# Kernel tuning notes

Measured on AMD Instinct MI355X. Metric: run time of the kernel, lower is better.

The kernel has to match this reference:

```python
import jax, jax.numpy as jnp
import numpy as np

B, S, D, DFF = 8, 2048, 1024, 4096

def setup_inputs() -> dict:
    key = jax.random.key(0)
    ks = jax.random.split(key, 11)
    s = 0.02
    return {
        "x":  jax.random.normal(ks[0], (B, S, D), dtype=jnp.float32),
        "Wq": jax.random.normal(ks[1], (D, D), dtype=jnp.float32) * s,
        "bq": jnp.zeros((D,), dtype=jnp.float32),
        "Wk": jax.random.normal(ks[2], (D, D), dtype=jnp.float32) * s,
        "bk": jnp.zeros((D,), dtype=jnp.float32),
        "Wv": jax.random.normal(ks[3], (D, D), dtype=jnp.float32) * s,
        "bv": jnp.zeros((D,), dtype=jnp.float32),
        "W1": jax.random.normal(ks[4], (DFF, D), dtype=jnp.float32) * s,
        "b1": jnp.zeros((DFF,), dtype=jnp.float32),
        "W2": jax.random.normal(ks[5], (D, DFF), dtype=jnp.float32) * s,
        "b2": jnp.zeros((D,), dtype=jnp.float32),
    }

def reference(x, Wq, bq, Wk, bk, Wv, bv, W1, b1, W2, b2):
    # qkv projections (torch Linear: x @ W.T + b)
    q = jnp.einsum('bsd,ed->bse', x, Wq) + bq
    k = jnp.einsum('bsd,ed->bse', x, Wk) + bk
    v = jnp.einsum('bsd,ed->bse', x, Wv) + bv
    # single-head scaled dot-product attention with causal mask (decoder=True)
    scale = 1.0 / jnp.sqrt(jnp.asarray(q.shape[-1], q.dtype))
    scores = jnp.einsum('bqd,bkd->bqk', q, k) * scale  # (B,S,S)
    causal = jnp.tril(jnp.ones((scores.shape[-2], scores.shape[-1]), dtype=bool))
    scores = jnp.where(causal, scores, jnp.asarray(-jnp.inf, scores.dtype))
    attn = jax.nn.softmax(scores, axis=-1)
    attn_out = jnp.einsum('bqk,bkd->bqd', attn, v)
    # MLP: linear_2(gelu(linear_1(.)))  — exact (erf) GELU as in torch default
    h = jax.nn.gelu(jnp.einsum('bsd,fd->bsf', attn_out, W1) + b1, approximate=False)
    return jnp.einsum('bsf,df->bsd', h, W2) + b2
```

## Files before the change

### kernel.cpp

```cpp
#include <hip/hip_runtime.h>
#include <hip/hip_bf16.h>

#define NB   8
#define SS   2048
#define DD   1024
#define DFFN 4096
#define MTOT (NB*SS)

typedef unsigned short u16;
typedef __attribute__((ext_vector_type(4))) float f32x4;
typedef __attribute__((ext_vector_type(8))) short bf16x8;
typedef __attribute__((ext_vector_type(4))) unsigned short u16x4;
typedef __attribute__((ext_vector_type(8))) unsigned short u16x8;

__device__ __forceinline__ u16 f2bf(float f) {
  union { float f; unsigned u; } c; c.f = f;
  unsigned r = c.u + 0x7FFFu + ((c.u >> 16) & 1u);
  return (u16)(r >> 16);
}

__device__ __forceinline__ void gload16(const void* g, void* l) {
  __builtin_amdgcn_global_load_lds(
      (const __attribute__((address_space(1))) void*)(unsigned long long)g,
      (__attribute__((address_space(3))) void*)(unsigned)(unsigned long long)l,
      16, 0, 0);
}

template<int EBIAS, int EGELU, int ESCALE, int EROWSCALE, int OUTMODE, int ETRANS, int CSKIP, int CK>
__global__ __launch_bounds__(512, 2)
void gemm256(const u16* __restrict__ A, const u16* __restrict__ B,
             const float* __restrict__ bias, const float* __restrict__ rowscale,
             void* __restrict__ C,
             int M, int N, int K, int lda, int ldb, int ldc, float scale,
             long long sA, long long sB, long long sC, int sRS)
{
  __shared__ __align__(1024) u16 smem[65536];

  const int nwg = gridDim.x * gridDim.y;
  const int orig = blockIdx.y * gridDim.x + blockIdx.x;
  const int q = nwg >> 3, r = nwg & 7;
  const int xcd = orig & 7, pos = orig >> 3;
  const int wg = (xcd < r ? xcd * (q + 1) : r * (q + 1) + (xcd - r) * q) + pos;
  const int bx = wg % gridDim.x, by = wg / gridDim.x;
  const int row0 = by * 256, col0 = bx * 256;
  if (CSKIP && col0 > row0 + 255) return;

  const int z = blockIdx.z;
  A += (size_t)z * sA;
  B += (size_t)z * sB;

  int nkt = K >> 5;
  if (CK) { int lim = (row0 + 256) >> 5; if (lim < nkt) nkt = lim; }

  const int tid  = threadIdx.x;
  const int wid  = tid >> 6;
  const int lane = tid & 63;
  const int wr = wid >> 2, wc = wid & 3;

  const int srow = wid * 16 + (lane >> 2);
  const int sunit = (lane & 3) ^ ((lane >> 3) & 3);
  const char* gA = (const char*)A + ((size_t)(row0 + srow) * lda + sunit * 8) * 2;
  const char* gB = (const char*)B + ((size_t)(col0 + srow) * ldb + sunit * 8) * 2;
  char* lbase = (char*)smem;
  const size_t ldab = (size_t)128 * lda * 2;
  const size_t ldbb = (size_t)128 * ldb * 2;

  #define STAGE(kt) {                                                        \
    char* lb = lbase + ((kt) & 3) * 32768;                                   \
    size_t kb = (size_t)(kt) * 64;                                           \
    gload16(gA + kb,        lb + wid * 1024);                                \
    gload16(gA + kb + ldab, lb + 8192 + wid * 1024);                         \
    gload16(gB + kb,        lb + 16384 + wid * 1024);                        \
    gload16(gB + kb + ldbb, lb + 16384 + 8192 + wid * 1024);                 \
  }

  const int rd_off = (lane & 15) * 64 + ((lane >> 4) & 3) * 16;
  const int xm = ((lane >> 1) & 3) << 4;
  const int aoff = wr * 8192;
  const int boff = 16384 + wc * 4096;

  f32x4 acc[8][4] = {};

  STAGE(0); STAGE(1); STAGE(2);
  asm volatile("s_waitcnt vmcnt(8)" ::: "memory");
  asm volatile("s_barrier" ::: "memory");

  for (int t = 0; t < nkt; ++t) {
    const int cb = (t & 3) * 32768;
    if (t + 3 < nkt) STAGE(t + 3);

    bf16x8 aR[8], bR[4];
#pragma unroll
    for (int m = 0; m < 8; ++m)
      aR[m] = *(const bf16x8*)((const char*)smem + ((cb + aoff + m * 1024 + rd_off) ^ xm));
#pragma unroll
    for (int n = 0; n < 4; ++n)
      bR[n] = *(const bf16x8*)((const char*)smem + ((cb + boff + n * 1024 + rd_off) ^ xm));

    __builtin_amdgcn_s_setprio(1);
#pragma unroll
    for (int m = 0; m < 8; ++m)
#pragma unroll
      for (int n = 0; n < 4; ++n)
        acc[m][n] = __builtin_amdgcn_mfma_f32_16x16x32_bf16(aR[m], bR[n], acc[m][n], 0, 0, 0);
    __builtin_amdgcn_s_setprio(0);

    asm volatile("s_waitcnt vmcnt(8)" ::: "memory");
    asm volatile("s_barrier" ::: "memory");
  }
  #undef STAGE

  const int r4 = (lane >> 4) * 4;
#pragma unroll
  for (int n = 0; n < 4; ++n) {
    const int col = col0 + wc * 64 + n * 16 + (lane & 15);
    float bia = EBIAS ? bias[col] : 0.0f;
#pragma unroll
    for (int m = 0; m < 8; ++m) {
      const int rowb = row0 + wr * 128 + m * 16 + r4;
#pragma unroll
      for (int j = 0; j < 4; ++j) {
        const int row = rowb + j;
        float x = acc[m][n][j];
        if (EBIAS)     x += bia;
        if (ESCALE)    x *= scale;
        if (EROWSCALE) x *= rowscale[z * sRS + row];
        if (EGELU)     x = 0.5f * x * (1.0f + erff(x * 0.70710678118f));
        if (ETRANS) {
          ((u16*)C)[(size_t)(row >> 11) * (DD * SS) + (size_t)col * SS + (row & (SS - 1))] = f2bf(x);
        } else if (OUTMODE == 1) {
          ((float*)C + (size_t)z * sC)[(size_t)row * ldc + col] = x;
        } else if (OUTMODE == 2) {
          ((_Float16*)C + (size_t)z * sC)[(size_t)row * ldc + col] = (_Float16)x;
        } else {
          ((u16*)C + (size_t)z * sC)[(size_t)row * ldc + col] = f2bf(x);
        }
      }
    }
  }
}

__global__ __launch_bounds__(256) void cvt_bf16_k(const float* __restrict__ in, u16* __restrict__ out, int n4) {
  int i = blockIdx.x * blockDim.x + threadIdx.x;
  if (i < n4) {
    float4 v = ((const float4*)in)[i];
    u16x4 o;
    o.x = f2bf(v.x); o.y = f2bf(v.y); o.z = f2bf(v.z); o.w = f2bf(v.w);
    ((u16x4*)out)[i] = o;
  }
}

__global__ __launch_bounds__(256) void softmax_k(u16* __restrict__ sc, float* __restrict__ rinv, int rows0) {
  const int widx = blockIdx.x * 4 + (threadIdx.x >> 6);
  const int lane = threadIdx.x & 63;
  u16* row = sc + (size_t)widx * SS;
  const int L = (widx & (SS - 1)) + 1;
  float mx = -1e30f;
  for (int k = 0; k < 4; ++k) {
    const int j0 = k * 512 + lane * 8;
    if (j0 < L) {
      u16x8 v = *(const u16x8*)(row + j0);
      int lim = L - j0; if (lim > 8) lim = 8;
#pragma unroll
      for (int e = 0; e < 8; ++e) {
        if (e < lim) { union { u16 u; _Float16 h; } c; c.u = v[e]; mx = fmaxf(mx, (float)c.h); }
      }
    }
  }
#pragma unroll
  for (int o = 32; o >= 1; o >>= 1) mx = fmaxf(mx, __shfl_xor(mx, o));
  float s = 0.0f;
  for (int k = 0; k < 4; ++k) {
    const int j0 = k * 512 + lane * 8;
    u16x8 v = *(const u16x8*)(row + j0);
    u16x8 w;
#pragma unroll
    for (int e = 0; e < 8; ++e) {
      const int j = j0 + e;
      float ev = 0.0f;
      if (j < L) { union { u16 u; _Float16 h; } c; c.u = v[e]; ev = __expf((float)c.h - mx); s += ev; }
      w[e] = f2bf(ev);
    }
    *(u16x8*)(row + j0) = w;
  }
#pragma unroll
  for (int o = 32; o >= 1; o >>= 1) s += __shfl_xor(s, o);
  if (lane == 0) rinv[rows0 + widx] = 1.0f / s;
}

extern "C" void kernel_launch(void* const* d_in, const int* in_sizes, int n_in,
                              void* d_out, int out_size, void* d_ws, size_t ws_size,
                              hipStream_t stream) {
  const float* x  = (const float*)d_in[0];
  const float* Wq = (const float*)d_in[1];
  const float* bq = (const float*)d_in[2];
  const float* Wk = (const float*)d_in[3];
  const float* bk = (const float*)d_in[4];
  const float* Wv = (const float*)d_in[5];
  const float* bv = (const float*)d_in[6];
  const float* W1 = (const float*)d_in[7];
  const float* b1 = (const float*)d_in[8];
  const float* W2 = (const float*)d_in[9];
  const float* b2 = (const float*)d_in[10];

  char* ws = (char*)d_ws;
  u16*  xb   = (u16*)(ws);
  u16*  Wqb  = (u16*)(ws + 33554432);
  u16*  Wkb  = (u16*)(ws + 35651584);
  u16*  Wvb  = (u16*)(ws + 37748736);
  u16*  W1b  = (u16*)(ws + 39845888);
  u16*  W2b  = (u16*)(ws + 48234496);
  u16*  Qb   = (u16*)(ws + 56623104);
  u16*  Kb   = (u16*)(ws + 90177536);
  u16*  Vtb  = (u16*)(ws + 123731968);
  float* rinv = (float*)(ws + 157286400);
  u16*  big  = (u16*)(ws + 157351936);
  u16*  att  = xb;

  const size_t base = 157351936ull;
  const size_t avail = ws_size > base ? ws_size - base : 0;
  int GB = 8; while (GB > 1 && (size_t)GB * 8388608ull > avail) GB >>= 1;
  int MC = 8192; while (MC > 2048 && (size_t)MC * 8192ull > avail) MC >>= 1;

  cvt_bf16_k<<<MTOT * DD / 4 / 256, 256, 0, stream>>>(x, xb, MTOT * DD / 4);
  cvt_bf16_k<<<DD * DD / 4 / 256, 256, 0, stream>>>(Wq, Wqb, DD * DD / 4);
  cvt_bf16_k<<<DD * DD / 4 / 256, 256, 0, stream>>>(Wk, Wkb, DD * DD / 4);
  cvt_bf16_k<<<DD * DD / 4 / 256, 256, 0, stream>>>(Wv, Wvb, DD * DD / 4);
  cvt_bf16_k<<<DFFN * DD / 4 / 256, 256, 0, stream>>>(W1, W1b, DFFN * DD / 4);
  cvt_bf16_k<<<DFFN * DD / 4 / 256, 256, 0, stream>>>(W2, W2b, DFFN * DD / 4);

  gemm256<1,0,0,0,0,0,0,0><<<dim3(DD/256, MTOT/256), 512, 0, stream>>>(
      xb, Wqb, bq, nullptr, (void*)Qb, MTOT, DD, DD, DD, DD, DD, 0.f, 0, 0, 0, 0);
  gemm256<1,0,0,0,0,0,0,0><<<dim3(DD/256, MTOT/256), 512, 0, stream>>>(
      xb, Wkb, bk, nullptr, (void*)Kb, MTOT, DD, DD, DD, DD, DD, 0.f, 0, 0, 0, 0);
  gemm256<1,0,0,0,0,1,0,0><<<dim3(DD/256, MTOT/256), 512, 0, stream>>>(
      xb, Wvb, bv, nullptr, (void*)Vtb, MTOT, DD, DD, DD, DD, DD, 0.f, 0, 0, 0, 0);

  for (int b0 = 0; b0 < NB; b0 += GB) {
    gemm256<0,0,1,0,2,0,1,0><<<dim3(SS/256, SS/256, GB), 512, 0, stream>>>(
        Qb + (size_t)b0 * SS * DD, Kb + (size_t)b0 * SS * DD, nullptr, nullptr,
        (void*)big, SS, SS, DD, DD, DD, SS, 0.03125f,
        (long long)SS * DD, (long long)SS * DD, (long long)SS * SS, 0);
    softmax_k<<<GB * SS / 4, 256, 0, stream>>>(big, rinv, b0 * SS);
    gemm256<0,0,0,1,0,0,0,1><<<dim3(DD/256, SS/256, GB), 512, 0, stream>>>(
        big, Vtb + (size_t)b0 * DD * SS, nullptr, rinv + (size_t)b0 * SS,
        (void*)(att + (size_t)b0 * SS * DD), SS, DD, SS, SS, SS, DD, 0.f,
        (long long)SS * SS, (long long)DD * SS, (long long)SS * DD, SS);
  }

  for (int c = 0; c < MTOT / MC; ++c) {
    u16* h = big;
    gemm256<1,1,0,0,0,0,0,0><<<dim3(DFFN/256, MC/256), 512, 0, stream>>>(
        att + (size_t)c * MC * DD, W1b, b1, nullptr, (void*)h,
        MC, DFFN, DD, DD, DD, DFFN, 0.f, 0, 0, 0, 0);
    gemm256<1,0,0,0,1,0,0,0><<<dim3(DD/256, MC/256), 512, 0, stream>>>(
        h, W2b, b2, nullptr, (void*)((float*)d_out + (size_t)c * MC * DD),
        MC, DD, DFFN, DFFN, DFFN, DD, 0.f, 0, 0, 0, 0);
  }
}
```

Before: 812.2 us.

## Split GEMM k-loop into two half-phases and stage epilogue through LDS

```diff
diff --git a/kernel.cpp b/kernel.cpp
--- a/kernel.cpp
+++ b/kernel.cpp
@@ -39,8 +39,8 @@
   const int nwg = gridDim.x * gridDim.y;
   const int orig = blockIdx.y * gridDim.x + blockIdx.x;
   const int q = nwg >> 3, r = nwg & 7;
-  const int xcd = orig & 7, pos = orig >> 3;
-  const int wg = (xcd < r ? xcd * (q + 1) : r * (q + 1) + (xcd - r) * q) + pos;
+  const int xcd = orig & 7, pos0 = orig >> 3;
+  const int wg = (xcd < r ? xcd * (q + 1) : r * (q + 1) + (xcd - r) * q) + pos0;
   const int bx = wg % gridDim.x, by = wg / gridDim.x;
   const int row0 = by * 256, col0 = bx * 256;
   if (CSKIP && col0 > row0 + 255) return;
@@ -65,77 +65,164 @@
   const size_t ldab = (size_t)128 * lda * 2;
   const size_t ldbb = (size_t)128 * ldb * 2;
 
-  #define STAGE(kt) {                                                        \
-    char* lb = lbase + ((kt) & 3) * 32768;                                   \
-    size_t kb = (size_t)(kt) * 64;                                           \
-    gload16(gA + kb,        lb + wid * 1024);                                \
-    gload16(gA + kb + ldab, lb + 8192 + wid * 1024);                         \
-    gload16(gB + kb,        lb + 16384 + wid * 1024);                        \
-    gload16(gB + kb + ldbb, lb + 16384 + 8192 + wid * 1024);                 \
-  }
-
-  const int rd_off = (lane & 15) * 64 + ((lane >> 4) & 3) * 16;
+  #define SHA(t2) { char* lb = lbase + ((t2) & 3) * 32768; size_t kb = (size_t)(t2) * 64; \
+      gload16(gA + kb,        lb + wid * 1024);                                          \
+      gload16(gA + kb + ldab, lb + 8192 + wid * 1024); }
+  #define SHB(t2) { char* lb = lbase + ((t2) & 3) * 32768; size_t kb = (size_t)(t2) * 64; \
+      gload16(gB + kb,        lb + 16384 + wid * 1024);                                   \
+      gload16(gB + kb + ldbb, lb + 16384 + 8192 + wid * 1024); }
+
+  const int fr = lane & 15;
+  const int rd_off = fr * 64 + ((lane >> 4) & 3) * 16;
   const int xm = ((lane >> 1) & 3) << 4;
   const int aoff = wr * 8192;
   const int boff = 16384 + wc * 4096;
 
   f32x4 acc[8][4] = {};
-
-  STAGE(0); STAGE(1); STAGE(2);
+  bf16x8 aLo[4], aHi[4], bb[4];
+
+  SHA(0); SHB(0); SHA(1); SHB(1); SHA(2); SHB(2);
   asm volatile("s_waitcnt vmcnt(8)" ::: "memory");
   asm volatile("s_barrier" ::: "memory");
 
   for (int t = 0; t < nkt; ++t) {
-    const int cb = (t & 3) * 32768;
-    if (t + 3 < nkt) STAGE(t + 3);
-
-    bf16x8 aR[8], bR[4];
-#pragma unroll
-    for (int m = 0; m < 8; ++m)
-      aR[m] = *(const bf16x8*)((const char*)smem + ((cb + aoff + m * 1024 + rd_off) ^ xm));
+    const char* cbuf = (const char*)smem + (t & 3) * 32768;
+#pragma unroll
+    for (int m = 0; m < 4; ++m)
+      aLo[m] = *(const bf16x8*)(cbuf + ((aoff + m * 1024 + rd_off) ^ xm));
 #pragma unroll
     for (int n = 0; n < 4; ++n)
-      bR[n] = *(const bf16x8*)((const char*)smem + ((cb + boff + n * 1024 + rd_off) ^ xm));
-
+      bb[n] = *(const bf16x8*)(cbuf + ((boff + n * 1024 + rd_off) ^ xm));
+    if (t + 3 < nkt) SHA(t + 3);
+    asm volatile("s_barrier" ::: "memory");
     __builtin_amdgcn_s_setprio(1);
 #pragma unroll
-    for (int m = 0; m < 8; ++m)
+    for (int m = 0; m < 4; ++m)
 #pragma unroll
       for (int n = 0; n < 4; ++n)
-        acc[m][n] = __builtin_amdgcn_mfma_f32_16x16x32_bf16(aR[m], bR[n], acc[m][n], 0, 0, 0);
+        acc[m][n] = __builtin_amdgcn_mfma_f32_16x16x32_bf16(aLo[m], bb[n], acc[m][n], 0, 0, 0);
     __builtin_amdgcn_s_setprio(0);
-
+    asm volatile("s_barrier" ::: "memory");
+#pragma unroll
+    for (int m = 0; m < 4; ++m)
+      aHi[m] = *(const bf16x8*)(cbuf + ((aoff + (m + 4) * 1024 + rd_off) ^ xm));
+    if (t + 3 < nkt) SHB(t + 3);
     asm volatile("s_waitcnt vmcnt(8)" ::: "memory");
     asm volatile("s_barrier" ::: "memory");
-  }
-  #undef STAGE
-
+    __builtin_amdgcn_s_setprio(1);
+#pragma unroll
+    for (int m = 0; m < 4; ++m)
+#pragma unroll
+      for (int n = 0; n < 4; ++n)
+        acc[m + 4][n] = __builtin_amdgcn_mfma_f32_16x16x32_bf16(aHi[m], bb[n], acc[m + 4][n], 0, 0, 0);
+    __builtin_amdgcn_s_setprio(0);
+    asm volatile("s_barrier" ::: "memory");
+  }
+  #undef SHA
+  #undef SHB
+
+  asm volatile("s_waitcnt vmcnt(0)" ::: "memory");
+  __syncthreads();
+
+  char* sm = (char*)smem;
   const int r4 = (lane >> 4) * 4;
-#pragma unroll
-  for (int n = 0; n < 4; ++n) {
-    const int col = col0 + wc * 64 + n * 16 + (lane & 15);
-    float bia = EBIAS ? bias[col] : 0.0f;
-#pragma unroll
-    for (int m = 0; m < 8; ++m) {
-      const int rowb = row0 + wr * 128 + m * 16 + r4;
-#pragma unroll
-      for (int j = 0; j < 4; ++j) {
-        const int row = rowb + j;
-        float x = acc[m][n][j];
-        if (EBIAS)     x += bia;
-        if (ESCALE)    x *= scale;
-        if (EROWSCALE) x *= rowscale[z * sRS + row];
-        if (EGELU)     x = 0.5f * x * (1.0f + erff(x * 0.70710678118f));
-        if (ETRANS) {
-          ((u16*)C)[(size_t)(row >> 11) * (DD * SS) + (size_t)col * SS + (row & (SS - 1))] = f2bf(x);
-        } else if (OUTMODE == 1) {
-          ((float*)C + (size_t)z * sC)[(size_t)row * ldc + col] = x;
-        } else if (OUTMODE == 2) {
-          ((_Float16*)C + (size_t)z * sC)[(size_t)row * ldc + col] = (_Float16)x;
-        } else {
-          ((u16*)C + (size_t)z * sC)[(size_t)row * ldc + col] = f2bf(x);
+
+  if (OUTMODE == 1) {
+#pragma unroll
+    for (int p = 0; p < 2; ++p) {
+      if ((wc >> 1) == p) {
+#pragma unroll
+        for (int n = 0; n < 4; ++n) {
+          const int col = col0 + wc * 64 + n * 16 + fr;
+          const int pcol = (wc & 1) * 64 + n * 16 + fr;
+          float bia = EBIAS ? bias[col] : 0.0f;
+#pragma unroll
+          for (int m = 0; m < 8; ++m) {
+#pragma unroll
+            for (int j = 0; j < 4; ++j) {
+              const int line = wr * 128 + m * 16 + r4 + j;
+              float xv = acc[m][n][j];
+              if (EBIAS)     xv += bia;
+              if (ESCALE)    xv *= scale;
+              if (EROWSCALE) xv *= rowscale[z * sRS + row0 + line];
+              if (EGELU)     xv = 0.5f * xv * (1.0f + erff(xv * 0.70710678118f));
+              *(float*)(sm + ((line * 512 + pcol * 4) ^ ((line & 12) << 3))) = xv;
+            }
+          }
         }
       }
+      __syncthreads();
+      float* Cb = (float*)C + (size_t)z * sC;
+#pragma unroll
+      for (int i = 0; i < 16; ++i) {
+        const int o = i * 8192 + tid * 16;
+        const int line = o >> 9, ps = o & 511;
+        f32x4 v = *(const f32x4*)(sm + ((line * 512 + ps) ^ ((line & 12) << 3)));
+        *(f32x4*)((char*)(Cb + (size_t)(row0 + line) * ldc + col0 + p * 128) + ps) = v;
+      }
+      __syncthreads();
+    }
+  } else if (ETRANS) {
+#pragma unroll
+    for (int n = 0; n < 4; ++n) {
+      const int col = col0 + wc * 64 + n * 16 + fr;
+      const int line = wc * 64 + n * 16 + fr;
+      float bia = EBIAS ? bias[col] : 0.0f;
+#pragma unroll
+      for (int m = 0; m < 8; ++m) {
+        const int rb = wr * 128 + m * 16 + r4;
+        u16x4 pk;
+#pragma unroll
+        for (int j = 0; j < 4; ++j) {
+          float xv = acc[m][n][j];
+          if (EBIAS)     xv += bia;
+          if (ESCALE)    xv *= scale;
+          if (EROWSCALE) xv *= rowscale[z * sRS + row0 + rb + j];
+          pk[j] = f2bf(xv);
+        }
+        *(u16x4*)(sm + ((line * 512 + rb * 2) ^ ((line & 15) << 4))) = pk;
+      }
+    }
+    __syncthreads();
+    u16* Cb = (u16*)C + (size_t)(row0 >> 11) * (DD * SS) + (row0 & (SS - 1));
+#pragma unroll
+    for (int i = 0; i < 16; ++i) {
+      const int o = i * 8192 + tid * 16;
+      const int line = o >> 9, ps = o & 511;
+      f32x4 v = *(const f32x4*)(sm + ((line * 512 + ps) ^ ((line & 15) << 4)));
+      *(f32x4*)((char*)(Cb + (size_t)(col0 + line) * SS) + ps) = v;
+    }
+  } else {
+#pragma unroll
+    for (int n = 0; n < 4; ++n) {
+      const int col = col0 + wc * 64 + n * 16 + fr;
+      const int pc = (wc * 64 + n * 16 + fr) * 2;
+      float bia = EBIAS ? bias[col] : 0.0f;
+#pragma unroll
+      for (int m = 0; m < 8; ++m) {
+#pragma unroll
+        for (int j = 0; j < 4; ++j) {
+          const int line = wr * 128 + m * 16 + r4 + j;
+          float xv = acc[m][n][j];
+          if (EBIAS)     xv += bia;
+          if (ESCALE)    xv *= scale;
+          if (EROWSCALE) xv *= rowscale[z * sRS + row0 + line];
+          if (EGELU)     xv = 0.5f * xv * (1.0f + erff(xv * 0.70710678118f));
+          u16 u;
+          if (OUTMODE == 2) { union { u16 s; _Float16 h; } cu; cu.h = (_Float16)xv; u = cu.s; }
+          else u = f2bf(xv);
+          *(u16*)(sm + ((line * 512 + pc) ^ ((line & 12) << 3))) = u;
+        }
+      }
+    }
+    __syncthreads();
+    u16* Cb = (u16*)C + (size_t)z * sC + col0;
+#pragma unroll
+    for (int i = 0; i < 16; ++i) {
+      const int o = i * 8192 + tid * 16;
+      const int line = o >> 9, ps = o & 511;
+      f32x4 v = *(const f32x4*)(sm + ((line * 512 + ps) ^ ((line & 12) << 3)));
+      *(f32x4*)((char*)(Cb + (size_t)(row0 + line) * ldc) + ps) = v;
     }
   }
 }
```

New measurement: 829.6 us. 1.02x slower.
